# Kernel tuning notes

Hardware: AMD Instinct MI355X
Metric: run time of the kernel (lower is better)

## Reference

```python
import jax, jax.numpy as jnp
import numpy as np

B, T, C, HD = 4, 2048, 1024, 64

def setup_inputs() -> dict:
    key = jax.random.key(0)
    kx, kq, kk, kv = jax.random.split(key, 4)
    # Weights stored as [n_embed, head_size]; equivalent to torch Linear weight transposed.
    scale = 1.0 / np.sqrt(C)
    return {
        "x": jax.random.normal(kx, (B, T, C), dtype=jnp.float32),
        "Wq": jax.random.normal(kq, (C, HD), dtype=jnp.float32) * scale,
        "Wk": jax.random.normal(kk, (C, HD), dtype=jnp.float32) * scale,
        "Wv": jax.random.normal(kv, (C, HD), dtype=jnp.float32) * scale,
    }

def reference(x, Wq, Wk, Wv):
    # Projections (no bias)
    q = x @ Wq  # [B,T,HD]
    k = x @ Wk
    v = x @ Wv
    hd = k.shape[-1]
    # NOTE: original multiplies by sqrt(head_size) (not the usual 1/sqrt) -- faithful.
    scores = jnp.einsum("btd,bsd->bts", q, k) * (hd ** 0.5)  # [B,T,T]
    # First softmax over full (unmasked) rows
    w = jax.nn.softmax(scores, axis=-1)
    # Causal mask applied AFTER the first softmax, then a second softmax
    causal = jnp.tril(jnp.ones((q.shape[1], q.shape[1]), dtype=bool))  # [T,T]
    w = jnp.where(causal[None, :, :], w, -jnp.inf)
    w = jax.nn.softmax(w, axis=-1)
    out = jnp.einsum("bts,bsd->btd", w, v)  # [B,T,HD]
    return out
```

## Files before the change

### kernel.cpp

```cpp
#include <hip/hip_runtime.h>
#include <math.h>

#define T_  2048
#define C_  1024
#define HD_ 64

typedef __attribute__((ext_vector_type(8))) short bf16x8;
typedef __attribute__((ext_vector_type(4))) float f32x4;

#define MFMA_BF16(A, B, C) __builtin_amdgcn_mfma_f32_16x16x32_bf16(A, B, C, 0, 0, 0)

__device__ __forceinline__ short f2bf(float f) {
    union { float f; unsigned u; } v; v.f = f;
    unsigned r = v.u + 0x7fffu + ((v.u >> 16) & 1u);
    return (short)(r >> 16);
}
__device__ __forceinline__ float bf2f(short s) {
    union { float f; unsigned u; } v;
    v.u = ((unsigned)(unsigned short)s) << 16;
    return v.f;
}

__global__ __launch_bounds__(256) void prep_w_kernel(
    const float* __restrict__ Wq, const float* __restrict__ Wk,
    const float* __restrict__ Wv, short* __restrict__ wtf)
{
    const int m = blockIdx.y;
    const float* W = (m == 0) ? Wq : (m == 1) ? Wk : Wv;
    const int t = threadIdx.x;
    const int c = blockIdx.x * 64 + (t >> 2);
    const int hg = (t & 3) * 16;
    const int ct = m * 4 + (t & 3);
    const int c0i = c >> 6, kc = (c >> 5) & 1, lq = (c >> 3) & 3, e = c & 7;
    const float4* wp = (const float4*)(W + (size_t)c * HD_ + hg);
    #pragma unroll
    for (int u = 0; u < 4; ++u) {
        float4 f = wp[u];
        float vs[4] = {f.x, f.y, f.z, f.w};
        #pragma unroll
        for (int ei = 0; ei < 4; ++ei) {
            int h16 = u * 4 + ei;
            int L = h16 + 16 * lq;
            short hh = f2bf(vs[ei]);
            short lo = f2bf(vs[ei] - bf2f(hh));
            size_t oh = ((((size_t)(ct * 2 + 0) * 16 + c0i) * 2 + kc) * 64 + L) * 8 + e;
            size_t ol = ((((size_t)(ct * 2 + 1) * 16 + c0i) * 2 + kc) * 64 + L) * 8 + e;
            wtf[oh] = hh;
            wtf[ol] = lo;
        }
    }
}

__global__ __launch_bounds__(512) void qkv_proj_kernel(
    const float* __restrict__ x, const short* __restrict__ wtf,
    short* __restrict__ qhp, short* __restrict__ qlp,
    short* __restrict__ khp, short* __restrict__ klp,
    short* __restrict__ vtp)
{
    __shared__ __align__(16) short xh[32 * 64], xl[32 * 64];

    const int t = threadIdx.x, L = t & 63, wv = t >> 6;
    const int R0 = blockIdx.x * 32;
    const int rtb = (wv >> 2) * 16;
    const int ctq = wv & 3;

    f32x4 acc[3];
    #pragma unroll
    for (int j = 0; j < 3; ++j) acc[j] = {0.f, 0.f, 0.f, 0.f};

    const int xrow = t >> 4, xc4 = t & 15;
    const float* xp = x + (size_t)(R0 + xrow) * C_ + xc4 * 4;
    float4 xa;
    auto loadX = [&](int c0) { xa = *(const float4*)(xp + c0); };

    const size_t lo8 = (size_t)L * 8;
    auto loadWF = [&](int c0i, int kc, bf16x8* w) {
        w[0] = *(const bf16x8*)(wtf + (size_t)((((ctq + 0) * 2 + 0) * 16 + c0i) * 2 + kc) * 512 + lo8);
        w[1] = *(const bf16x8*)(wtf + (size_t)((((ctq + 0) * 2 + 1) * 16 + c0i) * 2 + kc) * 512 + lo8);
        w[2] = *(const bf16x8*)(wtf + (size_t)((((ctq + 4) * 2 + 0) * 16 + c0i) * 2 + kc) * 512 + lo8);
        w[3] = *(const bf16x8*)(wtf + (size_t)((((ctq + 4) * 2 + 1) * 16 + c0i) * 2 + kc) * 512 + lo8);
        w[4] = *(const bf16x8*)(wtf + (size_t)((((ctq + 8) * 2 + 0) * 16 + c0i) * 2 + kc) * 512 + lo8);
    };

    bf16x8 wf0[5], wf1[5];
    loadX(0);
    loadWF(0, 0, wf0);

    const int c8 = xc4 >> 1, xhalf = xc4 & 1;
    const int arow = rtb + (L & 15);

    for (int c0i = 0; c0i < 16; ++c0i) {
        __syncthreads();
        {
            float vs[4] = {xa.x, xa.y, xa.z, xa.w};
            short4 vh, vl;
            short* vhp = (short*)&vh; short* vlp = (short*)&vl;
            #pragma unroll
            for (int e = 0; e < 4; ++e) {
                short hh = f2bf(vs[e]);
                vhp[e] = hh;
                vlp[e] = f2bf(vs[e] - bf2f(hh));
            }
            int slot = xrow * 64 + ((c8 ^ (xrow & 7)) * 8) + xhalf * 4;
            *(short4*)&xh[slot] = vh;
            *(short4*)&xl[slot] = vl;
        }
        if (c0i < 15) loadX((c0i + 1) * 64);
        __syncthreads();

        loadWF(c0i, 1, wf1);
        {
            int ch = 0 * 4 + (L >> 4);
            int off = arow * 64 + ((ch ^ (arow & 7)) * 8);
            bf16x8 axh = *(const bf16x8*)&xh[off];
            bf16x8 axl = *(const bf16x8*)&xl[off];
            acc[0] = MFMA_BF16(axl, wf0[0], acc[0]);
            acc[0] = MFMA_BF16(axh, wf0[1], acc[0]);
            acc[0] = MFMA_BF16(axh, wf0[0], acc[0]);
            acc[1] = MFMA_BF16(axl, wf0[2], acc[1]);
            acc[1] = MFMA_BF16(axh, wf0[3], acc[1]);
            acc[1] = MFMA_BF16(axh, wf0[2], acc[1]);
            acc[2] = MFMA_BF16(wf0[4], axh, acc[2]);
        }
        if (c0i < 15) loadWF(c0i + 1, 0, wf0);
        {
            int ch = 1 * 4 + (L >> 4);
            int off = arow * 64 + ((ch ^ (arow & 7)) * 8);
            bf16x8 axh = *(const bf16x8*)&xh[off];
            bf16x8 axl = *(const bf16x8*)&xl[off];
            acc[0] = MFMA_BF16(axl, wf1[0], acc[0]);
            acc[0] = MFMA_BF16(axh, wf1[1], acc[0]);
            acc[0] = MFMA_BF16(axh, wf1[0], acc[0]);
            acc[1] = MFMA_BF16(axl, wf1[2], acc[1]);
            acc[1] = MFMA_BF16(axh, wf1[3], acc[1]);
            acc[1] = MFMA_BF16(axh, wf1[2], acc[1]);
            acc[2] = MFMA_BF16(wf1[4], axh, acc[2]);
        }
    }

    const int quad = L >> 4;
    #pragma unroll
    for (int r = 0; r < 4; ++r) {
        int row = R0 + rtb + quad * 4 + r;
        int h = ctq * 16 + (L & 15);
        float vq = acc[0][r] * 8.f;
        short hq = f2bf(vq);
        qhp[(size_t)row * HD_ + h] = hq;
        qlp[(size_t)row * HD_ + h] = f2bf(vq - bf2f(hq));
        float vk = acc[1][r];
        short hk = f2bf(vk);
        khp[(size_t)row * HD_ + h] = hk;
        klp[(size_t)row * HD_ + h] = f2bf(vk - bf2f(hk));
        int d = ctq * 16 + quad * 4 + r;
        int tt = R0 + rtb + (L & 15);
        int bb = tt >> 11, tl = tt & (T_ - 1);
        vtp[(size_t)(bb * 64 + d) * T_ + tl] = f2bf(acc[2][r]);
    }
}

__global__ __launch_bounds__(256) void stats_kernel(
    const short* __restrict__ qhp, const short* __restrict__ qlp,
    const short* __restrict__ khp, const short* __restrict__ klp,
    float* __restrict__ pm, float* __restrict__ sc)
{
    __shared__ float red[4 * 64 * 2];

    const int t = threadIdx.x, L = t & 63, wv = t >> 6;
    const int bt = blockIdx.x, seg = blockIdx.y, b = blockIdx.z;
    const int R0 = bt * 64, S0 = seg * 256;

    bf16x8 qfh[4][2], qfl[4][2];
    #pragma unroll
    for (int rt = 0; rt < 4; ++rt)
        #pragma unroll
        for (int dc = 0; dc < 2; ++dc) {
            int row = R0 + rt * 16 + (L & 15);
            size_t off = ((size_t)b * T_ + row) * HD_ + dc * 32 + (L >> 4) * 8;
            qfh[rt][dc] = *(const bf16x8*)(qhp + off);
            qfl[rt][dc] = *(const bf16x8*)(qlp + off);
        }

    float ml[4][4], ll[4][4];
    #pragma unroll
    for (int rt = 0; rt < 4; ++rt)
        #pragma unroll
        for (int r = 0; r < 4; ++r) { ml[rt][r] = -1e30f; ll[rt][r] = 0.f; }

    const int colL = wv * 16 + (L & 15);
    const short* kbh = khp + ((size_t)b * T_ + S0 + colL) * HD_;
    const short* kbl = klp + ((size_t)b * T_ + S0 + colL) * HD_;
    const int cho = (L >> 4) * 8;

    bf16x8 kfh[2][2], kfl[2][2];
    auto loadK = [&](int jt, bf16x8 kh[2], bf16x8 kl[2]) {
        #pragma unroll
        for (int dc = 0; dc < 2; ++dc) {
            kh[dc] = *(const bf16x8*)(kbh + (size_t)jt * 64 * HD_ + dc * 32 + cho);
            kl[dc] = *(const bf16x8*)(kbl + (size_t)jt * 64 * HD_ + dc * 32 + cho);
        }
    };
    loadK(0, kfh[0], kfl[0]);

    #pragma unroll
    for (int jt = 0; jt < 4; ++jt) {
        const int cb = jt & 1;
        if (jt < 3) loadK(jt + 1, kfh[cb ^ 1], kfl[cb ^ 1]);
        const bool doStore = (S0 + jt * 64) <= (R0 + 63);
        #pragma unroll
        for (int rt = 0; rt < 4; ++rt) {
            f32x4 s = {0.f, 0.f, 0.f, 0.f};
            #pragma unroll
            for (int dc = 0; dc < 2; ++dc) {
                s = MFMA_BF16(qfl[rt][dc], kfh[cb][dc], s);
                s = MFMA_BF16(qfh[rt][dc], kfl[cb][dc], s);
                s = MFMA_BF16(qfh[rt][dc], kfh[cb][dc], s);
            }
            if (doStore) {
                #pragma unroll
                for (int r = 0; r < 4; ++r) {
                    int row = R0 + rt * 16 + (L >> 4) * 4 + r;
                    sc[((size_t)b * T_ + row) * T_ + S0 + jt * 64 + colL] = s[r];
                }
            }
            #pragma unroll
            for (int r = 0; r < 4; ++r) {
                float mn = fmaxf(ml[rt][r], s[r]);
                ll[rt][r] = ll[rt][r] * __expf(ml[rt][r] - mn) + __expf(s[r] - mn);
                ml[rt][r] = mn;
            }
        }
    }
    #pragma unroll
    for (int off = 1; off < 16; off <<= 1)
        #pragma unroll
        for (int rt = 0; rt < 4; ++rt)
            #pragma unroll
            for (int r = 0; r < 4; ++r) {
                float mo = __shfl_xor(ml[rt][r], off, 64);
                float lo = __shfl_xor(ll[rt][r], off, 64);
                float mn = fmaxf(ml[rt][r], mo);
                ll[rt][r] = ll[rt][r] * __expf(ml[rt][r] - mn) + lo * __expf(mo - mn);
                ml[rt][r] = mn;
            }
    if ((L & 15) == 0) {
        #pragma unroll
        for (int rt = 0; rt < 4; ++rt)
            #pragma unroll
            for (int r = 0; r < 4; ++r) {
                int row = rt * 16 + (L >> 4) * 4 + r;
                red[(wv * 64 + row) * 2 + 0] = ml[rt][r];
                red[(wv * 64 + row) * 2 + 1] = ll[rt][r];
            }
    }
    __syncthreads();
    if (t < 64) {
        float M = red[t * 2], S = red[t * 2 + 1];
        #pragma unroll
        for (int w = 1; w < 4; ++w) {
            float mo = red[(w * 64 + t) * 2], lo = red[(w * 64 + t) * 2 + 1];
            float mn = fmaxf(M, mo);
            S = S * __expf(M - mn) + lo * __expf(mo - mn);
            M = mn;
        }
        size_t o = ((size_t)((b * 32 + bt) * 8 + seg) * 64 + t) * 2;
        pm[o] = M;
        pm[o + 1] = S;
    }
}

__global__ __launch_bounds__(256) void pv_kernel(
    const float* __restrict__ sc, const short* __restrict__ vtp,
    const float* __restrict__ pm, float* __restrict__ out)
{
    __shared__ float ored[4][16][64];
    __shared__ float dred[4][16];
    __shared__ float msl[16], isl[16];

    const int t = threadIdx.x, L = t & 63, wv = t >> 6;
    const int b = blockIdx.x & 3;
    const int i = blockIdx.x >> 2;
    const int p = (i < 64) ? (127 - i) : (i - 64);
    const int T0 = p * 16;

    if (t < 16) {
        int row = T0 + t;
        int bt = row >> 6, rr = row & 63;
        float M = -1e30f, S = 0.f;
        #pragma unroll
        for (int seg = 0; seg < 8; ++seg) {
            size_t o = ((size_t)((b * 32 + bt) * 8 + seg) * 64 + rr) * 2;
            float mo = pm[o], lo = pm[o + 1];
            float mn = fmaxf(M, mo);
            S = S * __expf(M - mn) + lo * __expf(mo - mn);
            M = mn;
        }
        msl[t] = M;
        isl[t] = 1.f / S;
    }
    __syncthreads();

    const int row = T0 + (L & 15);
    const float ms = msl[L & 15];
    const float is = isl[L & 15];
    const float* srow = sc + ((size_t)b * T_ + row) * T_;
    const short* vb = vtp + (size_t)b * 64 * T_;
    const int nJ = (T0 + 143) >> 7;
    const int cq = (L >> 4) * 8;

    f32x4 ov[4];
    #pragma unroll
    for (int dt = 0; dt < 4; ++dt) ov[dt] = {0.f, 0.f, 0.f, 0.f};
    float dn = 0.f;

    for (int jt = 0; jt < nJ; ++jt) {
        const int c0 = jt * 128 + wv * 32 + cq;
        float4 s0 = *(const float4*)(srow + c0);
        float4 s1 = *(const float4*)(srow + c0 + 4);
        float vs[8] = {s0.x, s0.y, s0.z, s0.w, s1.x, s1.y, s1.z, s1.w};
        bf16x8 ef;
        #pragma unroll
        for (int e = 0; e < 8; ++e) {
            float pvv = __expf(vs[e] - ms) * is;
            float evv = (c0 + e <= row) ? __expf(pvv) : 0.f;
            dn += evv;
            ef[e] = f2bf(evv);
        }
        #pragma unroll
        for (int dt = 0; dt < 4; ++dt) {
            bf16x8 vf = *(const bf16x8*)(vb + (size_t)(dt * 16 + (L & 15)) * T_ + c0);
            ov[dt] = MFMA_BF16(ef, vf, ov[dt]);
        }
    }

    dn += __shfl_xor(dn, 16, 64);
    dn += __shfl_xor(dn, 32, 64);
    if (L < 16) dred[wv][L] = dn;
    #pragma unroll
    for (int dt = 0; dt < 4; ++dt)
        #pragma unroll
        for (int r = 0; r < 4; ++r)
            ored[wv][(L >> 4) * 4 + r][dt * 16 + (L & 15)] = ov[dt][r];
    __syncthreads();

    const int orow = t >> 4, d0 = (t & 15) * 4;
    float D = dred[0][orow] + dred[1][orow] + dred[2][orow] + dred[3][orow];
    float di = 1.f / D;
    float4 o;
    o.x = (ored[0][orow][d0 + 0] + ored[1][orow][d0 + 0]
         + ored[2][orow][d0 + 0] + ored[3][orow][d0 + 0]) * di;
    o.y = (ored[0][orow][d0 + 1] + ored[1][orow][d0 + 1]
         + ored[2][orow][d0 + 1] + ored[3][orow][d0 + 1]) * di;
    o.z = (ored[0][orow][d0 + 2] + ored[1][orow][d0 + 2]
         + ored[2][orow][d0 + 2] + ored[3][orow][d0 + 2]) * di;
    o.w = (ored[0][orow][d0 + 3] + ored[1][orow][d0 + 3]
         + ored[2][orow][d0 + 3] + ored[3][orow][d0 + 3]) * di;
    *(float4*)(out + ((size_t)b * T_ + T0 + orow) * HD_ + d0) = o;
}

extern "C" void kernel_launch(void* const* d_in, const int* in_sizes, int n_in,
                              void* d_out, int out_size, void* d_ws, size_t ws_size,
                              hipStream_t stream) {
    (void)in_sizes; (void)n_in; (void)out_size; (void)ws_size;
    const float* x  = (const float*)d_in[0];
    const float* Wq = (const float*)d_in[1];
    const float* Wk = (const float*)d_in[2];
    const float* Wv = (const float*)d_in[3];
    float* outp = (float*)d_out;

    char* ws = (char*)d_ws;
    short* wt  = (short*)ws;
    float* pm  = (float*)ws;
    short* qh = (short*)(ws + 786432);
    short* ql = (short*)(ws + 786432 + 1048576);
    short* kh = (short*)(ws + 786432 + 2 * 1048576);
    short* kl = (short*)(ws + 786432 + 3 * 1048576);
    short* vt = (short*)(ws + 786432 + 4 * 1048576);
    float* sc = (float*)(ws + 8388608);

    prep_w_kernel<<<dim3(16, 3), 256, 0, stream>>>(Wq, Wk, Wv, wt);
    qkv_proj_kernel<<<dim3(256), 512, 0, stream>>>(x, wt, qh, ql, kh, kl, vt);
    stats_kernel<<<dim3(32, 8, 4), 256, 0, stream>>>(qh, ql, kh, kl, pm, sc);
    pv_kernel<<<dim3(512), 256, 0, stream>>>(sc, vt, pm, outp);
}
```

Measured before the change: 139.9 us.

## Double-buffer x staging in QKV projection, prefetch scores/V in PV loop, fold softmax scale

```diff
diff --git a/kernel.cpp b/kernel.cpp
--- a/kernel.cpp
+++ b/kernel.cpp
@@ -51,18 +51,17 @@
     }
 }
 
-__global__ __launch_bounds__(512) void qkv_proj_kernel(
+__global__ __launch_bounds__(256) void qkv_proj_kernel(
     const float* __restrict__ x, const short* __restrict__ wtf,
     short* __restrict__ qhp, short* __restrict__ qlp,
     short* __restrict__ khp, short* __restrict__ klp,
     short* __restrict__ vtp)
 {
-    __shared__ __align__(16) short xh[32 * 64], xl[32 * 64];
+    __shared__ __align__(16) short xh[2][16 * 64], xl[2][16 * 64];
 
     const int t = threadIdx.x, L = t & 63, wv = t >> 6;
-    const int R0 = blockIdx.x * 32;
-    const int rtb = (wv >> 2) * 16;
-    const int ctq = wv & 3;
+    const int R0 = blockIdx.x * 16;
+    const int ctq = wv;
 
     f32x4 acc[3];
     #pragma unroll
@@ -72,6 +71,22 @@
     const float* xp = x + (size_t)(R0 + xrow) * C_ + xc4 * 4;
     float4 xa;
     auto loadX = [&](int c0) { xa = *(const float4*)(xp + c0); };
+
+    const int c8 = xc4 >> 1, xhalf = xc4 & 1;
+    const int slot = xrow * 64 + ((c8 ^ (xrow & 7)) * 8) + xhalf * 4;
+    auto stageX = [&](int buf) {
+        float vs[4] = {xa.x, xa.y, xa.z, xa.w};
+        short4 vh, vl;
+        short* vhp = (short*)&vh; short* vlp = (short*)&vl;
+        #pragma unroll
+        for (int e = 0; e < 4; ++e) {
+            short hh = f2bf(vs[e]);
+            vhp[e] = hh;
+            vlp[e] = f2bf(vs[e] - bf2f(hh));
+        }
+        *(short4*)&xh[buf][slot] = vh;
+        *(short4*)&xl[buf][slot] = vl;
+    };
 
     const size_t lo8 = (size_t)L * 8;
     auto loadWF = [&](int c0i, int kc, bf16x8* w) {
@@ -83,37 +98,26 @@
     };
 
     bf16x8 wf0[5], wf1[5];
+    const int arow = L & 15;
+
     loadX(0);
     loadWF(0, 0, wf0);
-
-    const int c8 = xc4 >> 1, xhalf = xc4 & 1;
-    const int arow = rtb + (L & 15);
+    stageX(0);
+    loadX(64);
+    __syncthreads();
 
     for (int c0i = 0; c0i < 16; ++c0i) {
-        __syncthreads();
-        {
-            float vs[4] = {xa.x, xa.y, xa.z, xa.w};
-            short4 vh, vl;
-            short* vhp = (short*)&vh; short* vlp = (short*)&vl;
-            #pragma unroll
-            for (int e = 0; e < 4; ++e) {
-                short hh = f2bf(vs[e]);
-                vhp[e] = hh;
-                vlp[e] = f2bf(vs[e] - bf2f(hh));
-            }
-            int slot = xrow * 64 + ((c8 ^ (xrow & 7)) * 8) + xhalf * 4;
-            *(short4*)&xh[slot] = vh;
-            *(short4*)&xl[slot] = vl;
-        }
-        if (c0i < 15) loadX((c0i + 1) * 64);
-        __syncthreads();
-
+        const int cur = c0i & 1;
+        if (c0i < 15) {
+            stageX(cur ^ 1);
+            if (c0i < 14) loadX((c0i + 2) * 64);
+        }
         loadWF(c0i, 1, wf1);
         {
             int ch = 0 * 4 + (L >> 4);
             int off = arow * 64 + ((ch ^ (arow & 7)) * 8);
-            bf16x8 axh = *(const bf16x8*)&xh[off];
-            bf16x8 axl = *(const bf16x8*)&xl[off];
+            bf16x8 axh = *(const bf16x8*)&xh[cur][off];
+            bf16x8 axl = *(const bf16x8*)&xl[cur][off];
             acc[0] = MFMA_BF16(axl, wf0[0], acc[0]);
             acc[0] = MFMA_BF16(axh, wf0[1], acc[0]);
             acc[0] = MFMA_BF16(axh, wf0[0], acc[0]);
@@ -126,8 +130,8 @@
         {
             int ch = 1 * 4 + (L >> 4);
             int off = arow * 64 + ((ch ^ (arow & 7)) * 8);
-            bf16x8 axh = *(const bf16x8*)&xh[off];
-            bf16x8 axl = *(const bf16x8*)&xl[off];
+            bf16x8 axh = *(const bf16x8*)&xh[cur][off];
+            bf16x8 axl = *(const bf16x8*)&xl[cur][off];
             acc[0] = MFMA_BF16(axl, wf1[0], acc[0]);
             acc[0] = MFMA_BF16(axh, wf1[1], acc[0]);
             acc[0] = MFMA_BF16(axh, wf1[0], acc[0]);
@@ -136,12 +140,13 @@
             acc[1] = MFMA_BF16(axh, wf1[2], acc[1]);
             acc[2] = MFMA_BF16(wf1[4], axh, acc[2]);
         }
+        __syncthreads();
     }
 
     const int quad = L >> 4;
     #pragma unroll
     for (int r = 0; r < 4; ++r) {
-        int row = R0 + rtb + quad * 4 + r;
+        int row = R0 + quad * 4 + r;
         int h = ctq * 16 + (L & 15);
         float vq = acc[0][r] * 8.f;
         short hq = f2bf(vq);
@@ -152,7 +157,7 @@
         khp[(size_t)row * HD_ + h] = hk;
         klp[(size_t)row * HD_ + h] = f2bf(vk - bf2f(hk));
         int d = ctq * 16 + quad * 4 + r;
-        int tt = R0 + rtb + (L & 15);
+        int tt = R0 + (L & 15);
         int bb = tt >> 11, tl = tt & (T_ - 1);
         vtp[(size_t)(bb * 64 + d) * T_ + tl] = f2bf(acc[2][r]);
     }
@@ -274,7 +279,7 @@
 {
     __shared__ float ored[4][16][64];
     __shared__ float dred[4][16];
-    __shared__ float msl[16], isl[16];
+    __shared__ float msl[16];
 
     const int t = threadIdx.x, L = t & 63, wv = t >> 6;
     const int b = blockIdx.x & 3;
@@ -294,14 +299,12 @@
             S = S * __expf(M - mn) + lo * __expf(mo - mn);
             M = mn;
         }
-        msl[t] = M;
-        isl[t] = 1.f / S;
+        msl[t] = M + __logf(S);
     }
     __syncthreads();
 
     const int row = T0 + (L & 15);
-    const float ms = msl[L & 15];
-    const float is = isl[L & 15];
+    const float mls = msl[L & 15];
     const float* srow = sc + ((size_t)b * T_ + row) * T_;
     const short* vb = vtp + (size_t)b * 64 * T_;
     const int nJ = (T0 + 143) >> 7;
@@ -312,25 +315,51 @@
     for (int dt = 0; dt < 4; ++dt) ov[dt] = {0.f, 0.f, 0.f, 0.f};
     float dn = 0.f;
 
-    for (int jt = 0; jt < nJ; ++jt) {
-        const int c0 = jt * 128 + wv * 32 + cq;
-        float4 s0 = *(const float4*)(srow + c0);
-        float4 s1 = *(const float4*)(srow + c0 + 4);
-        float vs[8] = {s0.x, s0.y, s0.z, s0.w, s1.x, s1.y, s1.z, s1.w};
-        bf16x8 ef;
-        #pragma unroll
-        for (int e = 0; e < 8; ++e) {
-            float pvv = __expf(vs[e] - ms) * is;
-            float evv = (c0 + e <= row) ? __expf(pvv) : 0.f;
-            dn += evv;
-            ef[e] = f2bf(evv);
-        }
-        #pragma unroll
-        for (int dt = 0; dt < 4; ++dt) {
-            bf16x8 vf = *(const bf16x8*)(vb + (size_t)(dt * 16 + (L & 15)) * T_ + c0);
-            ov[dt] = MFMA_BF16(ef, vf, ov[dt]);
-        }
-    }
+    float4 sa0, sa1, sb0, sb1;
+    bf16x8 va0, va1, va2, va3, vb0, vb1, vb2, vb3;
+
+#define LDS_(jt, s0, s1) { int c0_ = (jt) * 128 + wv * 32 + cq;                  \
+        s0 = *(const float4*)(srow + c0_); s1 = *(const float4*)(srow + c0_ + 4); }
+#define LDV_(jt, v0, v1, v2, v3) { int c0_ = (jt) * 128 + wv * 32 + cq;          \
+        v0 = *(const bf16x8*)(vb + (size_t)( 0 + (L & 15)) * T_ + c0_);          \
+        v1 = *(const bf16x8*)(vb + (size_t)(16 + (L & 15)) * T_ + c0_);          \
+        v2 = *(const bf16x8*)(vb + (size_t)(32 + (L & 15)) * T_ + c0_);          \
+        v3 = *(const bf16x8*)(vb + (size_t)(48 + (L & 15)) * T_ + c0_); }
+#define BODY_(jt, s0, s1, v0, v1, v2, v3) {                                      \
+        const int c0_ = (jt) * 128 + wv * 32 + cq;                               \
+        float vs_[8] = {s0.x, s0.y, s0.z, s0.w, s1.x, s1.y, s1.z, s1.w};         \
+        bf16x8 ef_;                                                              \
+        _Pragma("unroll")                                                        \
+        for (int e = 0; e < 8; ++e) {                                            \
+            float pvv = __expf(vs_[e] - mls);                                    \
+            float evv = (c0_ + e <= row) ? __expf(pvv) : 0.f;                    \
+            dn += evv;                                                           \
+            ef_[e] = f2bf(evv);                                                  \
+        }                                                                        \
+        ov[0] = MFMA_BF16(ef_, v0, ov[0]);                                       \
+        ov[1] = MFMA_BF16(ef_, v1, ov[1]);                                       \
+        ov[2] = MFMA_BF16(ef_, v2, ov[2]);                                       \
+        ov[3] = MFMA_BF16(ef_, v3, ov[3]); }
+
+    LDS_(0, sa0, sa1)
+    LDV_(0, va0, va1, va2, va3)
+    int jt = 0;
+    for (; jt + 2 <= nJ; jt += 2) {
+        LDS_(jt + 1, sb0, sb1)
+        LDV_(jt + 1, vb0, vb1, vb2, vb3)
+        BODY_(jt, sa0, sa1, va0, va1, va2, va3)
+        if (jt + 2 < nJ) {
+            LDS_(jt + 2, sa0, sa1)
+            LDV_(jt + 2, va0, va1, va2, va3)
+        }
+        BODY_(jt + 1, sb0, sb1, vb0, vb1, vb2, vb3)
+    }
+    if (jt < nJ) {
+        BODY_(jt, sa0, sa1, va0, va1, va2, va3)
+    }
+#undef LDS_
+#undef LDV_
+#undef BODY_
 
     dn += __shfl_xor(dn, 16, 64);
     dn += __shfl_xor(dn, 32, 64);
@@ -378,7 +407,7 @@
     float* sc = (float*)(ws + 8388608);
 
     prep_w_kernel<<<dim3(16, 3), 256, 0, stream>>>(Wq, Wk, Wv, wt);
-    qkv_proj_kernel<<<dim3(256), 512, 0, stream>>>(x, wt, qh, ql, kh, kl, vt);
+    qkv_proj_kernel<<<dim3(512), 256, 0, stream>>>(x, wt, qh, ql, kh, kl, vt);
     stats_kernel<<<dim3(32, 8, 4), 256, 0, stream>>>(qh, ql, kh, kl, pm, sc);
     pv_kernel<<<dim3(512), 256, 0, stream>>>(sc, vt, pm, outp);
 }
```

New measurement: 135.1 us. 3.4% less time.
